# Kernel optimization log

Measured on AMD Instinct MI355X. Metric: run time of the kernel, lower is better.

The kernel has to match this reference:

```python
import jax, jax.numpy as jnp
import numpy as np

B, S, H = 1, 1024, 2048          # batch, seq, hidden_size
I = 7168                          # intermediate_size
E = 8                             # num_local_experts
TOP_K = 2                         # num_experts_per_tok
R = int(I * H * 0.1 / (I + H))    # delta_low_rank = 159
SCALE = 0.02


def setup_inputs() -> dict:
    key = jax.random.key(0)
    ks = jax.random.split(key, 12)
    f = jnp.float32
    return {
        "x": jax.random.normal(ks[0], (B, S, H), dtype=f),
        "gate_w": jax.random.normal(ks[1], (E, H), dtype=f) * SCALE,
        "Wm1": jax.random.normal(ks[2], (I, H), dtype=f) * SCALE,  # Wmean1 (gate proj)
        "Wm2": jax.random.normal(ks[3], (H, I), dtype=f) * SCALE,  # Wmean2 (down proj)
        "Wm3": jax.random.normal(ks[4], (I, H), dtype=f) * SCALE,  # Wmean3 (up proj)
        "du1": jax.random.normal(ks[5], (E, I, R), dtype=f) * SCALE,
        "dv1": jax.random.normal(ks[6], (E, R, H), dtype=f) * SCALE,
        "du2": jax.random.normal(ks[7], (E, H, R), dtype=f) * SCALE,
        "dv2": jax.random.normal(ks[8], (E, R, I), dtype=f) * SCALE,
        "du3": jax.random.normal(ks[9], (E, I, R), dtype=f) * SCALE,
        "dv3": jax.random.normal(ks[10], (E, R, H), dtype=f) * SCALE,
    }


def reference(x, gate_w, Wm1, Wm2, Wm3, du1, dv1, du2, dv2, du3, dv3):
    b, s, h = x.shape
    hs = x.reshape(-1, h)                                  # [T, H]

    # --- router ---
    router_logits = hs @ gate_w.T                          # [T, E]
    probs = jax.nn.softmax(router_logits.astype(jnp.float32), axis=-1)
    top_w, top_i = jax.lax.top_k(probs, TOP_K)             # [T, K]
    top_w = top_w / jnp.sum(top_w, axis=-1, keepdims=True)
    # dense combine weights [T, E]: weight of expert e for token t (0 if not selected)
    comb = jnp.sum(jax.nn.one_hot(top_i, E, dtype=top_w.dtype) * top_w[..., None], axis=1)
    comb = comb.astype(hs.dtype)

    # --- shared mean weights (computed once per token) ---
    base_gate = hs @ Wm1.T                                 # [T, I]
    base_up = hs @ Wm3.T                                   # [T, I]

    # --- per-expert low-rank deltas ---
    t1 = jnp.einsum('th,erh->ter', hs, dv1)                # [T, E, R]
    gate = base_gate[:, None, :] + jnp.einsum('ter,eir->tei', t1, du1)  # [T, E, I]
    t3 = jnp.einsum('th,erh->ter', hs, dv3)
    up = base_up[:, None, :] + jnp.einsum('ter,eir->tei', t3, du3)      # [T, E, I]

    hmid = jax.nn.silu(gate) * up                          # [T, E, I]

    out = jnp.einsum('tei,hi->teh', hmid, Wm2)             # shared down proj
    t2 = jnp.einsum('tei,eri->ter', hmid, dv2)
    out = out + jnp.einsum('ter,ehr->teh', t2, du2)        # [T, E, H]

    final = jnp.einsum('te,teh->th', comb, out).reshape(b, s, h)
    return final, router_logits
```

## Files before the change

### kernel.cpp

```cpp
#include <hip/hip_runtime.h>

#define T_TOK 1024
#define H_DIM 2048
#define I_DIM 7168
#define E_NUM 8
#define R_RANK 159
#define RP 160
#define P_PAIRS 2048

typedef __attribute__((ext_vector_type(8))) short short8;
typedef __attribute__((ext_vector_type(4))) float f32x4;

__device__ __forceinline__ ushort f2b(float f) {
  uint u = __float_as_uint(f);
  uint r = (u + 0x7FFFu + ((u >> 16) & 1u)) >> 16;
  return (ushort)r;
}
__device__ __forceinline__ float b2f(ushort u) {
  return __uint_as_float(((uint)u) << 16);
}
__device__ __forceinline__ short8 pack8(float4 a, float4 b) {
  short8 o;
  o[0] = (short)f2b(a.x); o[1] = (short)f2b(a.y); o[2] = (short)f2b(a.z); o[3] = (short)f2b(a.w);
  o[4] = (short)f2b(b.x); o[5] = (short)f2b(b.y); o[6] = (short)f2b(b.z); o[7] = (short)f2b(b.w);
  return o;
}
__device__ __forceinline__ short8 zero8() {
  short8 z;
#pragma unroll
  for (int q = 0; q < 8; ++q) z[q] = 0;
  return z;
}
__device__ __forceinline__ int swzofs(int row, int g) { return (g ^ ((row >> 1) & 3)) * 8; }

#define GLOAD(gptr, lptr) \
  __builtin_amdgcn_global_load_lds((const __attribute__((address_space(1))) void*)(gptr), \
                                   (__attribute__((address_space(3))) void*)(lptr), 16, 0, 0)

__global__ __launch_bounds__(256) void router_kernel(
    const float* __restrict__ x, const float* __restrict__ gw,
    float* __restrict__ logits, float* __restrict__ comb,
    int* __restrict__ sel_e, int* __restrict__ cnt) {
  int wave = threadIdx.x >> 6, lane = threadIdx.x & 63;
  int t = blockIdx.x * 4 + wave;
  const float* xr = x + (long)t * H_DIM;
  float acc[8] = {0.f,0.f,0.f,0.f,0.f,0.f,0.f,0.f};
  for (int h = lane * 4; h < H_DIM; h += 256) {
    const float4 xv = *(const float4*)&xr[h];
#pragma unroll
    for (int e = 0; e < 8; ++e) {
      const float4 gv = *(const float4*)&gw[e * H_DIM + h];
      acc[e] += xv.x * gv.x + xv.y * gv.y + xv.z * gv.z + xv.w * gv.w;
    }
  }
#pragma unroll
  for (int off = 32; off > 0; off >>= 1)
#pragma unroll
    for (int e = 0; e < 8; ++e) acc[e] += __shfl_down(acc[e], off);
  if (lane == 0) {
#pragma unroll
    for (int e = 0; e < 8; ++e) logits[(long)t * 8 + e] = acc[e];
    int i0 = 0;
    for (int e = 1; e < 8; ++e) if (acc[e] > acc[i0]) i0 = e;
    int i1 = (i0 == 0) ? 1 : 0;
    for (int e = 0; e < 8; ++e) if (e != i0 && acc[e] > acc[i1]) i1 = e;
    float ee = __expf(acc[i1] - acc[i0]);
    float w0 = 1.f / (1.f + ee), w1 = ee / (1.f + ee);
    for (int e = 0; e < 8; ++e) comb[t * 8 + e] = 0.f;
    comb[t * 8 + i0] = w0;
    comb[t * 8 + i1] = w1;
    sel_e[t * 2] = i0;
    sel_e[t * 2 + 1] = i1;
    atomicAdd(&cnt[i0], 1);
    atomicAdd(&cnt[i1], 1);
  }
}

__global__ void init_kernel(int* cnt, int* cursor) {
  int i = threadIdx.x;
  if (i < 8) { cnt[i] = 0; cursor[i] = 0; }
}

__global__ void scan_kernel(const int* cnt, int* seg) {
  if (threadIdx.x == 0) {
    int s = 0;
    for (int e = 0; e < 8; ++e) { seg[e] = s; s += cnt[e]; }
    seg[8] = s;
  }
}

__global__ void assign_kernel(const int* __restrict__ sel_e, const float* __restrict__ comb,
                              const int* __restrict__ seg, int* __restrict__ cursor,
                              int* __restrict__ tok, float* __restrict__ wrow,
                              int* __restrict__ row_of) {
  int t = blockIdx.x * blockDim.x + threadIdx.x;
  if (t >= T_TOK) return;
  for (int k = 0; k < 2; ++k) {
    int e = sel_e[t * 2 + k];
    int pos = atomicAdd(&cursor[e], 1);
    int row = seg[e] + pos;
    tok[row] = t;
    wrow[row] = comb[t * 8 + e];
    row_of[t * 2 + k] = row;
  }
}

__global__ void cast8_kernel(const float* __restrict__ src, ushort* __restrict__ dst, long n8) {
  long idx = (long)blockIdx.x * blockDim.x + threadIdx.x;
  long stride = (long)gridDim.x * blockDim.x;
  for (long i = idx; i < n8; i += stride) {
    const float4 a = *(const float4*)&src[i * 8];
    const float4 b = *(const float4*)&src[i * 8 + 4];
    *(short8*)&dst[i * 8] = pack8(a, b);
  }
}

__global__ void padcast8_kernel(const float* __restrict__ src, ushort* __restrict__ dst, long rows) {
  long n8 = rows * (RP / 8);
  long idx = (long)blockIdx.x * blockDim.x + threadIdx.x;
  long stride = (long)gridDim.x * blockDim.x;
  for (long i = idx; i < n8; i += stride) {
    long row = i / (RP / 8);
    int c0 = (int)(i % (RP / 8)) * 8;
    short8 o;
#pragma unroll
    for (int j = 0; j < 8; ++j) {
      int c = c0 + j;
      o[j] = (c < R_RANK) ? (short)f2b(src[row * R_RANK + c]) : (short)0;
    }
    *(short8*)&dst[row * RP + c0] = o;
  }
}

__global__ void hcomb_kernel(const ushort* __restrict__ hmid, const int* __restrict__ row_of,
                             ushort* __restrict__ hc) {
  long idx = (long)blockIdx.x * blockDim.x + threadIdx.x;
  long total = (long)T_TOK * I_DIM / 8;
  if (idx >= total) return;
  long i = idx * 8;
  int t = (int)(i / I_DIM);
  int col = (int)(i % I_DIM);
  int r0 = row_of[t * 2], r1 = row_of[t * 2 + 1];
  const short8 a = *(const short8*)&hmid[(long)r0 * I_DIM + col];
  const short8 b = *(const short8*)&hmid[(long)r1 * I_DIM + col];
  short8 o;
#pragma unroll
  for (int j = 0; j < 8; ++j)
    o[j] = (short)f2b(b2f((ushort)a[j]) + b2f((ushort)b[j]));
  *(short8*)&hc[i] = o;
}

__global__ void finalfix_kernel(float* __restrict__ out, const ushort* __restrict__ delta,
                                const int* __restrict__ row_of) {
  long idx = (long)blockIdx.x * blockDim.x + threadIdx.x;
  long total = (long)T_TOK * H_DIM / 4;
  if (idx >= total) return;
  long i = idx * 4;
  int t = (int)(i / H_DIM);
  int col = (int)(i % H_DIM);
  int r0 = row_of[t * 2], r1 = row_of[t * 2 + 1];
  float4 d = *(float4*)&out[i];
  d.x += b2f(delta[(long)r0 * H_DIM + col + 0]) + b2f(delta[(long)r1 * H_DIM + col + 0]);
  d.y += b2f(delta[(long)r0 * H_DIM + col + 1]) + b2f(delta[(long)r1 * H_DIM + col + 1]);
  d.z += b2f(delta[(long)r0 * H_DIM + col + 2]) + b2f(delta[(long)r1 * H_DIM + col + 2]);
  d.w += b2f(delta[(long)r0 * H_DIM + col + 3]) + b2f(delta[(long)r1 * H_DIM + col + 3]);
  *(float4*)&out[i] = d;
}

__global__ void finalfixA_kernel(float* __restrict__ out, const float* __restrict__ dp,
                                 const ushort* __restrict__ delta, const int* __restrict__ row_of) {
  long idx = (long)blockIdx.x * blockDim.x + threadIdx.x;
  long total = (long)T_TOK * H_DIM / 4;
  if (idx >= total) return;
  long i = idx * 4;
  int t = (int)(i / H_DIM);
  int col = (int)(i % H_DIM);
  int r0 = row_of[t * 2], r1 = row_of[t * 2 + 1];
  const long plane = (long)T_TOK * H_DIM;
  float4 s = *(const float4*)&dp[i];
#pragma unroll
  for (int k = 1; k < 4; ++k) {
    const float4 q = *(const float4*)&dp[k * plane + i];
    s.x += q.x; s.y += q.y; s.z += q.z; s.w += q.w;
  }
  s.x += b2f(delta[(long)r0 * H_DIM + col + 0]) + b2f(delta[(long)r1 * H_DIM + col + 0]);
  s.y += b2f(delta[(long)r0 * H_DIM + col + 1]) + b2f(delta[(long)r1 * H_DIM + col + 1]);
  s.z += b2f(delta[(long)r0 * H_DIM + col + 2]) + b2f(delta[(long)r1 * H_DIM + col + 2]);
  s.w += b2f(delta[(long)r0 * H_DIM + col + 3]) + b2f(delta[(long)r1 * H_DIM + col + 3]);
  *(float4*)&out[i] = s;
}

template <int KS>
__global__ void reduce_cast_kernel(const float* __restrict__ P, long plane,
                                   ushort* __restrict__ out, long n) {
  long i = (long)blockIdx.x * blockDim.x + threadIdx.x;
  if (i >= n) return;
  float s = 0.f;
#pragma unroll
  for (int k = 0; k < KS; ++k) s += P[(long)k * plane + i];
  out[i] = f2b(s);
}

__global__ void reduce2_kernel(const float* __restrict__ p1, const float* __restrict__ p3,
                               ushort* __restrict__ t1g, ushort* __restrict__ t3g, long n) {
  long i = (long)blockIdx.x * blockDim.x + threadIdx.x;
  if (i >= 2 * n) return;
  const float* P = (i < n) ? p1 : p3;
  ushort* o = (i < n) ? t1g : t3g;
  long ii = (i < n) ? i : i - n;
  float s = 0.f;
#pragma unroll
  for (int k = 0; k < 8; ++k) s += P[(long)k * n + ii];
  o[ii] = f2b(s);
}


__device__ __forceinline__ void kloop32(
    const ushort* ar0, const ushort* ar1,
    const ushort* br0, const ushort* br1,
    int K, ushort* As, ushort* Bs,
    int tid, int lane, int wm, int wn, f32x4 acc[4][4]) {
  for (int k0 = 0; k0 < K; k0 += 32) {
    __syncthreads();
    GLOAD(ar0 + k0, &As[tid * 8]);
    GLOAD(ar1 + k0, &As[(256 + tid) * 8]);
    GLOAD(br0 + k0, &Bs[tid * 8]);
    GLOAD(br1 + k0, &Bs[(256 + tid) * 8]);
    __syncthreads();
    short8 av[4], bv[4];
#pragma unroll
    for (int mi = 0; mi < 4; ++mi) {
      int R = wm + mi * 16 + (lane & 15);
      av[mi] = *(const short8*)&As[R * 32 + swzofs(R, lane >> 4)];
    }
#pragma unroll
    for (int ni = 0; ni < 4; ++ni) {
      int R = wn + ni * 16 + (lane & 15);
      bv[ni] = *(const short8*)&Bs[R * 32 + swzofs(R, lane >> 4)];
    }
#pragma unroll
    for (int mi = 0; mi < 4; ++mi)
#pragma unroll
      for (int ni = 0; ni < 4; ++ni)
        acc[mi][ni] = __builtin_amdgcn_mfma_f32_16x16x32_bf16(av[mi], bv[ni], acc[mi][ni], 0, 0, 0);
  }
}

__device__ __forceinline__ void kloop64(
    const ushort* ar0, const ushort* ar1,
    const ushort* br0, const ushort* br1,
    int K, ushort* As, ushort* Bs,
    int tid, int lane, int wm, int wn, f32x4 acc[4][4]) {
  for (int k0 = 0; k0 < K; k0 += 64) {
    __syncthreads();
    GLOAD(ar0 + k0,      &As[tid * 8]);
    GLOAD(ar1 + k0,      &As[(256 + tid) * 8]);
    GLOAD(ar0 + k0 + 32, &As[4096 + tid * 8]);
    GLOAD(ar1 + k0 + 32, &As[4096 + (256 + tid) * 8]);
    GLOAD(br0 + k0,      &Bs[tid * 8]);
    GLOAD(br1 + k0,      &Bs[(256 + tid) * 8]);
    GLOAD(br0 + k0 + 32, &Bs[4096 + tid * 8]);
    GLOAD(br1 + k0 + 32, &Bs[4096 + (256 + tid) * 8]);
    __syncthreads();
#pragma unroll
    for (int s = 0; s < 2; ++s) {
      short8 av[4], bv[4];
#pragma unroll
      for (int mi = 0; mi < 4; ++mi) {
        int R = wm + mi * 16 + (lane & 15);
        av[mi] = *(const short8*)&As[s * 4096 + R * 32 + swzofs(R, lane >> 4)];
      }
#pragma unroll
      for (int ni = 0; ni < 4; ++ni) {
        int R = wn + ni * 16 + (lane & 15);
        bv[ni] = *(const short8*)&Bs[s * 4096 + R * 32 + swzofs(R, lane >> 4)];
      }
#pragma unroll
      for (int mi = 0; mi < 4; ++mi)
#pragma unroll
        for (int ni = 0; ni < 4; ++ni)
          acc[mi][ni] = __builtin_amdgcn_mfma_f32_16x16x32_bf16(av[mi], bv[ni], acc[mi][ni], 0, 0, 0);
    }
  }
}

__device__ __forceinline__ void epi_bf16(
    f32x4 acc[4][4], ushort* smem, int tid, int lane, int wm, int wn,
    int row0, int col0, int M, int Nvalid, int Npad, ushort* Cb, int ldc) {
  const int er = (lane >> 4) * 4, ec = lane & 15;
  __syncthreads();
#pragma unroll
  for (int mi = 0; mi < 4; ++mi)
#pragma unroll
    for (int ni = 0; ni < 4; ++ni)
#pragma unroll
      for (int j = 0; j < 4; ++j) {
        int rr = wm + mi * 16 + er + j;
        int c = wn + ni * 16 + ec;
        smem[rr * 128 + (c ^ ((rr & 7) << 3))] =
            (col0 + c < Nvalid) ? f2b(acc[mi][ni][j]) : (ushort)0;
      }
  __syncthreads();
  const int rl = tid >> 1, clb = (tid & 1) * 64;
  const int r = row0 + rl;
  if (r < M) {
    const int k8 = (rl & 7) << 3;
#pragma unroll
    for (int jj = 0; jj < 8; ++jj) {
      int cg = col0 + clb + jj * 8;
      if (cg < Npad) {
        short8 v = *(const short8*)&smem[rl * 128 + ((clb + jj * 8) ^ k8)];
        *(short8*)&Cb[(long)r * ldc + cg] = v;
      }
    }
  }
}


__global__ __launch_bounds__(256) void k_base(
    const ushort* __restrict__ xb, const ushort* __restrict__ w1b, const ushort* __restrict__ w3b,
    ushort* __restrict__ bgate, ushort* __restrict__ bup) {
  __shared__ ushort smem[16384];
  ushort* As = smem;
  ushort* Bs = smem + 8192;
  const ushort* B = blockIdx.z ? w3b : w1b;
  ushort* C = blockIdx.z ? bup : bgate;
  const int tid = threadIdx.x;
  const int lane = tid & 63, wave = tid >> 6;
  const int wm = (wave >> 1) * 64, wn = (wave & 1) * 64;
  const int row0 = blockIdx.y * 128, col0 = blockIdx.x * 128;
  const int sub_r = tid >> 2, sub_c = swzofs(sub_r, tid & 3);
  const ushort* ar0 = xb + (long)(row0 + sub_r) * H_DIM + sub_c;
  const ushort* ar1 = xb + (long)(row0 + 64 + sub_r) * H_DIM + sub_c;
  const ushort* br0 = B + (long)(col0 + sub_r) * H_DIM + sub_c;
  const ushort* br1 = B + (long)(col0 + 64 + sub_r) * H_DIM + sub_c;
  f32x4 acc[4][4] = {};
  kloop64(ar0, ar1, br0, br1, H_DIM, As, Bs, tid, lane, wm, wn, acc);
  epi_bf16(acc, smem, tid, lane, wm, wn, row0, col0, T_TOK, I_DIM, I_DIM, C, I_DIM);
}

__global__ __launch_bounds__(256) void k_t13(
    const ushort* __restrict__ xb, const ushort* __restrict__ dv1b, const ushort* __restrict__ dv3b,
    const int* __restrict__ tok, const int* __restrict__ seg, const int* __restrict__ cnt,
    float* __restrict__ p1, float* __restrict__ p3) {
  __shared__ ushort smem[16384];
  ushort* As = smem;
  ushort* Bs = smem + 8192;
  const int z = blockIdx.z;
  const int which = z & 1;
  const int eks = z >> 1;
  const int e = eks >> 3, ks = eks & 7;
  const int m0 = seg[e], M = cnt[e];
  const int row0 = blockIdx.y * 128, col0 = blockIdx.x * 128;
  if (row0 >= M) return;
  const int kbase = ks * 256;
  const ushort* Bsrc = (which ? dv3b : dv1b) + (long)e * R_RANK * H_DIM;
  float* P = which ? p3 : p1;
  const int tid = threadIdx.x;
  const int lane = tid & 63, wave = tid >> 6;
  const int wm = (wave >> 1) * 64, wn = (wave & 1) * 64;
  const int sub_r = tid >> 2, sub_c = swzofs(sub_r, tid & 3);
  int r0c = row0 + sub_r;      if (r0c > M - 1) r0c = M - 1;
  int r1c = row0 + 64 + sub_r; if (r1c > M - 1) r1c = M - 1;
  const ushort* ar0 = xb + (long)tok[m0 + r0c] * H_DIM + kbase + sub_c;
  const ushort* ar1 = xb + (long)tok[m0 + r1c] * H_DIM + kbase + sub_c;
  int q0 = col0 + sub_r;      if (q0 > R_RANK - 1) q0 = R_RANK - 1;
  int q1 = col0 + 64 + sub_r; if (q1 > R_RANK - 1) q1 = R_RANK - 1;
  const ushort* br0 = Bsrc + (long)q0 * H_DIM + kbase + sub_c;
  const ushort* br1 = Bsrc + (long)q1 * H_DIM + kbase + sub_c;
  f32x4 acc[4][4] = {};
  kloop64(ar0, ar1, br0, br1, 256, As, Bs, tid, lane, wm, wn, acc);
  const int er = (lane >> 4) * 4, ec = lane & 15;
  const long plane = (long)P_PAIRS * RP;
#pragma unroll
  for (int mi = 0; mi < 4; ++mi)
#pragma unroll
    for (int ni = 0; ni < 4; ++ni)
#pragma unroll
      for (int j = 0; j < 4; ++j) {
        int r = row0 + wm + mi * 16 + er + j;
        int c = col0 + wn + ni * 16 + ec;
        if (r < M && c < RP)
          P[(long)ks * plane + (long)(m0 + r) * RP + c] = (c < R_RANK) ? acc[mi][ni][j] : 0.f;
      }
}

__global__ __launch_bounds__(256) void k_phase2(
    const ushort* __restrict__ hc, const ushort* __restrict__ w2b,
    const ushort* __restrict__ hmidg, const ushort* __restrict__ dv2b,
    const int* __restrict__ seg, const int* __restrict__ cnt,
    float* __restrict__ dp, float* __restrict__ p2) {
  __shared__ ushort smem[16384];
  ushort* As = smem;
  ushort* Bs = smem + 8192;
  const int tid = threadIdx.x;
  const int lane = tid & 63, wave = tid >> 6;
  const int wm = (wave >> 1) * 64, wn = (wave & 1) * 64;
  const int sub_r = tid >> 2, sub_c = swzofs(sub_r, tid & 3);
  const int er = (lane >> 4) * 4, ec = lane & 15;

  if (blockIdx.z < 4) {
    const int ks = blockIdx.z;
    const int kbase = ks * (I_DIM / 4);
    const int row0 = blockIdx.y * 128, col0 = blockIdx.x * 128;
    const ushort* ar0 = hc + (long)(row0 + sub_r) * I_DIM + kbase + sub_c;
    const ushort* ar1 = hc + (long)(row0 + 64 + sub_r) * I_DIM + kbase + sub_c;
    const ushort* br0 = w2b + (long)(col0 + sub_r) * I_DIM + kbase + sub_c;
    const ushort* br1 = w2b + (long)(col0 + 64 + sub_r) * I_DIM + kbase + sub_c;
    f32x4 acc[4][4] = {};
    kloop64(ar0, ar1, br0, br1, I_DIM / 4, As, Bs, tid, lane, wm, wn, acc);
    float* Pk = dp + (long)ks * T_TOK * H_DIM;
#pragma unroll
    for (int mi = 0; mi < 4; ++mi)
#pragma unroll
      for (int ni = 0; ni < 4; ++ni)
#pragma unroll
        for (int j = 0; j < 4; ++j) {
          int r = row0 + wm + mi * 16 + er + j;
          int c = col0 + wn + ni * 16 + ec;
          Pk[(long)r * H_DIM + c] = acc[mi][ni][j];
        }
  } else {
    const int f = (blockIdx.z - 4) * 128 + blockIdx.y * 16 + blockIdx.x;
    const int eks = f >> 4;
    const int e = eks >> 3, ks = eks & 7;
    const int rsub = f & 15;
    const int x2 = rsub & 1, y2 = rsub >> 1;
    const int m0 = seg[e], M = cnt[e];
    const int row0 = y2 * 128, col0 = x2 * 128;
    if (row0 >= M) return;
    const int kbase = ks * (I_DIM / 8);
    int r0c = row0 + sub_r;      if (r0c > M - 1) r0c = M - 1;
    int r1c = row0 + 64 + sub_r; if (r1c > M - 1) r1c = M - 1;
    const ushort* ar0 = hmidg + (long)(m0 + r0c) * I_DIM + kbase + sub_c;
    const ushort* ar1 = hmidg + (long)(m0 + r1c) * I_DIM + kbase + sub_c;
    int q0 = col0 + sub_r;      if (q0 > R_RANK - 1) q0 = R_RANK - 1;
    int q1 = col0 + 64 + sub_r; if (q1 > R_RANK - 1) q1 = R_RANK - 1;
    const ushort* br0 = dv2b + (long)e * R_RANK * I_DIM + (long)q0 * I_DIM + kbase + sub_c;
    const ushort* br1 = dv2b + (long)e * R_RANK * I_DIM + (long)q1 * I_DIM + kbase + sub_c;
    f32x4 acc[4][4] = {};
    kloop64(ar0, ar1, br0, br1, I_DIM / 8, As, Bs, tid, lane, wm, wn, acc);
    const long plane = (long)P_PAIRS * RP;
#pragma unroll
    for (int mi = 0; mi < 4; ++mi)
#pragma unroll
      for (int ni = 0; ni < 4; ++ni)
#pragma unroll
        for (int j = 0; j < 4; ++j) {
          int r = row0 + wm + mi * 16 + er + j;
          int c = col0 + wn + ni * 16 + ec;
          if (r < M && c < RP)
            p2[(long)ks * plane + (long)(m0 + r) * RP + c] = (c < R_RANK) ? acc[mi][ni][j] : 0.f;
        }
  }
}

__global__ __launch_bounds__(256) void k_delta(
    const ushort* __restrict__ t2g, const ushort* __restrict__ du2b,
    const int* __restrict__ seg, const int* __restrict__ cnt,
    ushort* __restrict__ deltab) {
  __shared__ ushort smem[16384];
  ushort* As = smem;
  ushort* Bs = smem + 4096;
  const int e = blockIdx.z;
  const int m0 = seg[e], M = cnt[e];
  const int row0 = blockIdx.y * 128, col0 = blockIdx.x * 128;
  if (row0 >= M) return;
  const int tid = threadIdx.x;
  const int lane = tid & 63, wave = tid >> 6;
  const int wm = (wave >> 1) * 64, wn = (wave & 1) * 64;
  const int sub_r = tid >> 2, sub_c = swzofs(sub_r, tid & 3);
  int r0c = row0 + sub_r;      if (r0c > M - 1) r0c = M - 1;
  int r1c = row0 + 64 + sub_r; if (r1c > M - 1) r1c = M - 1;
  const ushort* ar0 = t2g + (long)(m0 + r0c) * RP + sub_c;
  const ushort* ar1 = t2g + (long)(m0 + r1c) * RP + sub_c;
  const ushort* br0 = du2b + (long)e * H_DIM * RP + (long)(col0 + sub_r) * RP + sub_c;
  const ushort* br1 = du2b + (long)e * H_DIM * RP + (long)(col0 + 64 + sub_r) * RP + sub_c;
  f32x4 acc[4][4] = {};
  kloop32(ar0, ar1, br0, br1, RP, As, Bs, tid, lane, wm, wn, acc);
  epi_bf16(acc, smem, tid, lane, wm, wn, row0, col0, M, H_DIM, H_DIM,
           deltab + (long)m0 * H_DIM, H_DIM);
}

__global__ __launch_bounds__(256) void gemm_hmid(
    const ushort* __restrict__ t1g, const ushort* __restrict__ t3g,
    const ushort* __restrict__ du1b, const ushort* __restrict__ du3b,
    const ushort* __restrict__ bgate, const ushort* __restrict__ bup,
    const int* __restrict__ tok, const float* __restrict__ wrow,
    const int* __restrict__ seg, const int* __restrict__ cnt,
    ushort* __restrict__ hmid) {
  __shared__ ushort smem[16384];
  ushort* As1 = smem;
  ushort* As3 = smem + 4096;
  ushort* Bs1 = smem + 8192;
  ushort* Bs3 = smem + 12288;
  int e = blockIdx.z;
  int m0 = seg[e], M = cnt[e];
  if ((int)(blockIdx.y * 128) >= M) return;
  const ushort* A1 = t1g + (long)m0 * RP;
  const ushort* A3 = t3g + (long)m0 * RP;
  const ushort* B1 = du1b + (long)e * I_DIM * RP;
  const ushort* B3 = du3b + (long)e * I_DIM * RP;
  tok += m0; wrow += m0;
  ushort* H = hmid + (long)m0 * I_DIM;

  const int tid = threadIdx.x;
  const int lane = tid & 63, wave = tid >> 6;
  const int wm = (wave >> 1) * 64, wn = (wave & 1) * 64;
  const int row0 = blockIdx.y * 128, col0 = blockIdx.x * 128;
  const int sub_r = tid >> 2;
  const int sub_c = swzofs(sub_r, tid & 3);

  const ushort *a1r[2], *a3r[2], *b1r[2], *b3r[2];
#pragma unroll
  for (int p = 0; p < 2; ++p) {
    int r = row0 + p * 64 + sub_r; if (r > M - 1) r = M - 1;
    a1r[p] = A1 + (long)r * RP + sub_c;
    a3r[p] = A3 + (long)r * RP + sub_c;
    int q = col0 + p * 64 + sub_r; if (q > I_DIM - 1) q = I_DIM - 1;
    b1r[p] = B1 + (long)q * RP + sub_c;
    b3r[p] = B3 + (long)q * RP + sub_c;
  }

  f32x4 acc1[4][4] = {}, acc3[4][4] = {};

  for (int k0 = 0; k0 < RP; k0 += 32) {
    __syncthreads();
#pragma unroll
    for (int p = 0; p < 2; ++p) {
      GLOAD(a1r[p] + k0, &As1[(p * 256 + tid) * 8]);
      GLOAD(a3r[p] + k0, &As3[(p * 256 + tid) * 8]);
      GLOAD(b1r[p] + k0, &Bs1[(p * 256 + tid) * 8]);
      GLOAD(b3r[p] + k0, &Bs3[(p * 256 + tid) * 8]);
    }
    __syncthreads();

    short8 av1[4], av3[4], bv1[4], bv3[4];
#pragma unroll
    for (int mi = 0; mi < 4; ++mi) {
      int R = wm + mi * 16 + (lane & 15);
      int o = R * 32 + swzofs(R, lane >> 4);
      av1[mi] = *(const short8*)&As1[o];
      av3[mi] = *(const short8*)&As3[o];
    }
#pragma unroll
    for (int ni = 0; ni < 4; ++ni) {
      int R = wn + ni * 16 + (lane & 15);
      int o = R * 32 + swzofs(R, lane >> 4);
      bv1[ni] = *(const short8*)&Bs1[o];
      bv3[ni] = *(const short8*)&Bs3[o];
    }
#pragma unroll
    for (int mi = 0; mi < 4; ++mi)
#pragma unroll
      for (int ni = 0; ni < 4; ++ni) {
        acc1[mi][ni] = __builtin_amdgcn_mfma_f32_16x16x32_bf16(av1[mi], bv1[ni], acc1[mi][ni], 0, 0, 0);
        acc3[mi][ni] = __builtin_amdgcn_mfma_f32_16x16x32_bf16(av3[mi], bv3[ni], acc3[mi][ni], 0, 0, 0);
      }
  }

  const int er = (lane >> 4) * 4;
  const int ec = lane & 15;
  __syncthreads();
  ushort* Cs = smem;
#pragma unroll
  for (int mi = 0; mi < 4; ++mi)
#pragma unroll
    for (int ni = 0; ni < 4; ++ni)
#pragma unroll
      for (int j = 0; j < 4; ++j) {
        int rr = wm + mi * 16 + er + j;
        int c = wn + ni * 16 + ec;
        Cs[rr * 128 + (c ^ ((rr & 7) << 3))] = f2b(acc1[mi][ni][j]);
      }
  __syncthreads();
  const int rl = tid >> 1;
  const int clb = (tid & 1) * 64;
  const int r = row0 + rl;
  const bool rok = (r < M);
  const int t = rok ? tok[r] : 0;
  const float w = rok ? wrow[r] : 0.f;
  const int k8 = (rl & 7) << 3;
  uint svp[32];
#pragma unroll
  for (int jj = 0; jj < 8; ++jj) {
    short8 gb = zero8();
    if (rok) gb = *(const short8*)&bgate[(long)t * I_DIM + col0 + clb + jj * 8];
    short8 gv = *(const short8*)&Cs[rl * 128 + ((clb + jj * 8) ^ k8)];
#pragma unroll
    for (int q = 0; q < 8; q += 2) {
      float g0 = b2f((ushort)gv[q]) + b2f((ushort)gb[q]);
      float g1 = b2f((ushort)gv[q + 1]) + b2f((ushort)gb[q + 1]);
      float s0 = g0 / (1.f + __expf(-g0));
      float s1 = g1 / (1.f + __expf(-g1));
      svp[jj * 4 + q / 2] = (uint)f2b(s0) | ((uint)f2b(s1) << 16);
    }
  }
  __syncthreads();
#pragma unroll
  for (int mi = 0; mi < 4; ++mi)
#pragma unroll
    for (int ni = 0; ni < 4; ++ni)
#pragma unroll
      for (int j = 0; j < 4; ++j) {
        int rr = wm + mi * 16 + er + j;
        int c = wn + ni * 16 + ec;
        Cs[rr * 128 + (c ^ ((rr & 7) << 3))] = f2b(acc3[mi][ni][j]);
      }
  __syncthreads();
#pragma unroll
  for (int jj = 0; jj < 8; ++jj) {
    short8 ub = zero8();
    if (rok) ub = *(const short8*)&bup[(long)t * I_DIM + col0 + clb + jj * 8];
    short8 uv = *(const short8*)&Cs[rl * 128 + ((clb + jj * 8) ^ k8)];
    short8 o;
#pragma unroll
    for (int q = 0; q < 8; q += 2) {
      uint sp = svp[jj * 4 + q / 2];
      float u0 = b2f((ushort)uv[q]) + b2f((ushort)ub[q]);
      float u1 = b2f((ushort)uv[q + 1]) + b2f((ushort)ub[q + 1]);
      o[q]     = (short)f2b(w * b2f((ushort)(sp & 0xFFFFu)) * u0);
      o[q + 1] = (short)f2b(w * b2f((ushort)(sp >> 16)) * u1);
    }
    if (rok) *(short8*)&H[(long)r * I_DIM + col0 + clb + jj * 8] = o;
  }
}

template <int AF32, int BF32, int CBF16, int PEREXP, int AMAP>
__global__ __launch_bounds__(256) void gemm_f(
    const void* __restrict__ Ap, int lda,
    const void* __restrict__ Bp, int ldb, long Bstride,
    int M, int N, int K, int Npad,
    float* __restrict__ Cf, ushort* __restrict__ Cb, int ldc,
    const int* __restrict__ tok, const int* __restrict__ seg, const int* __restrict__ cnt) {
  __shared__ ushort smem[16384];
  ushort* As = smem;
  ushort* Bs = smem + 4096;
  const float* Af = (const float*)Ap;
  const ushort* Ab = (const ushort*)Ap;
  const float* Bf = (const float*)Bp;
  const ushort* Bb = (const ushort*)Bp;
  const int* amap = tok;
  if (PEREXP) {
    int e = blockIdx.z;
    int m0 = seg[e];
    M = cnt[e];
    if ((int)(blockIdx.y * 128) >= M) return;
    if (AMAP) {
      amap = tok + m0;
    } else {
      if (AF32) Af += (long)m0 * lda; else Ab += (long)m0 * lda;
    }
    if (BF32) Bf += (long)e * Bstride; else Bb += (long)e * Bstride;
    if (CBF16) Cb += (long)m0 * ldc; else Cf += (long)m0 * ldc;
  }
  const int tid = threadIdx.x;
  const int lane = tid & 63, wave = tid >> 6;
  const int wm = (wave >> 1) * 64, wn = (wave & 1) * 64;
  const int row0 = blockIdx.y * 128, col0 = blockIdx.x * 128;
  const int sub_r = tid >> 2;
  const int sub_c = (tid & 3) * 8;

  const float* afrow[2]; const ushort* abrow[2];
  const float* bfrow[2]; const ushort* bbrow[2];
#pragma unroll
  for (int p = 0; p < 2; ++p) {
    int r = row0 + p * 64 + sub_r; if (r > M - 1) r = M - 1;
    if (AMAP) r = amap[r];
    if (AF32) afrow[p] = Af + (long)r * lda + sub_c;
    else      abrow[p] = Ab + (long)r * lda + sub_c;
    int q = col0 + p * 64 + sub_r; if (q > N - 1) q = N - 1;
    if (BF32) bfrow[p] = Bf + (long)q * ldb + sub_c;
    else      bbrow[p] = Bb + (long)q * ldb + sub_c;
  }

  f32x4 acc[4][4] = {};

  for (int k0 = 0; k0 < K; k0 += 32) {
    float4 a0[2], a1[2], b0[2], b1[2];
    if (AF32) {
#pragma unroll
      for (int p = 0; p < 2; ++p) {
        a0[p] = *(const float4*)(afrow[p] + k0);
        a1[p] = *(const float4*)(afrow[p] + k0 + 4);
      }
    }
    if (BF32) {
#pragma unroll
      for (int p = 0; p < 2; ++p) {
        b0[p] = *(const float4*)(bfrow[p] + k0);
        b1[p] = *(const float4*)(bfrow[p] + k0 + 4);
      }
    }
    __syncthreads();
#pragma unroll
    for (int p = 0; p < 2; ++p) {
      if (AF32) {
        *(short8*)&As[(p * 256 + tid) * 8] = pack8(a0[p], a1[p]);
      } else {
        GLOAD(abrow[p] + k0, &As[(p * 256 + tid) * 8]);
      }
      if (BF32) {
        *(short8*)&Bs[(p * 256 + tid) * 8] = pack8(b0[p], b1[p]);
      } else {
        GLOAD(bbrow[p] + k0, &Bs[(p * 256 + tid) * 8]);
      }
    }
    __syncthreads();

    short8 av[4], bv[4];
#pragma unroll
    for (int mi = 0; mi < 4; ++mi)
      av[mi] = *(const short8*)&As[(wm + mi * 16 + (lane & 15)) * 32 + (lane >> 4) * 8];
#pragma unroll
    for (int ni = 0; ni < 4; ++ni)
      bv[ni] = *(const short8*)&Bs[(wn + ni * 16 + (lane & 15)) * 32 + (lane >> 4) * 8];
#pragma unroll
    for (int mi = 0; mi < 4; ++mi)
#pragma unroll
      for (int ni = 0; ni < 4; ++ni)
        acc[mi][ni] = __builtin_amdgcn_mfma_f32_16x16x32_bf16(av[mi], bv[ni], acc[mi][ni], 0, 0, 0);
  }

  const int er = (lane >> 4) * 4;
  const int ec = lane & 15;
  if (CBF16) {
    __syncthreads();
    ushort* Cs = smem;
#pragma unroll
    for (int mi = 0; mi < 4; ++mi)
#pragma unroll
      for (int ni = 0; ni < 4; ++ni)
#pragma unroll
        for (int j = 0; j < 4; ++j) {
          int rr = wm + mi * 16 + er + j;
          int c = wn + ni * 16 + ec;
          Cs[rr * 128 + (c ^ ((rr & 7) << 3))] =
              (col0 + c < N) ? f2b(acc[mi][ni][j]) : (ushort)0;
        }
    __syncthreads();
    const int rl = tid >> 1;
    const int clb = (tid & 1) * 64;
    const int r = row0 + rl;
    if (r < M) {
      const int k8 = (rl & 7) << 3;
#pragma unroll
      for (int jj = 0; jj < 8; ++jj) {
        int cg = col0 + clb + jj * 8;
        if (cg < Npad) {
          short8 v = *(const short8*)&Cs[rl * 128 + ((clb + jj * 8) ^ k8)];
          *(short8*)&Cb[(long)r * ldc + cg] = v;
        }
      }
    }
  } else {
#pragma unroll
    for (int mi = 0; mi < 4; ++mi)
#pragma unroll
      for (int ni = 0; ni < 4; ++ni)
#pragma unroll
        for (int j = 0; j < 4; ++j) {
          int r = row0 + wm + mi * 16 + er + j;
          int c = col0 + wn + ni * 16 + ec;
          if (r < M && c < Npad)
            Cf[(long)r * ldc + c] = (c < N) ? acc[mi][ni][j] : 0.f;
        }
  }
}

extern "C" void kernel_launch(void* const* d_in, const int* in_sizes, int n_in,
                              void* d_out, int out_size, void* d_ws, size_t ws_size,
                              hipStream_t stream) {
  const float* x   = (const float*)d_in[0];
  const float* gw  = (const float*)d_in[1];
  const float* Wm1 = (const float*)d_in[2];
  const float* Wm2 = (const float*)d_in[3];
  const float* Wm3 = (const float*)d_in[4];
  const float* du1 = (const float*)d_in[5];
  const float* dv1 = (const float*)d_in[6];
  const float* du2 = (const float*)d_in[7];
  const float* dv2 = (const float*)d_in[8];
  const float* du3 = (const float*)d_in[9];
  const float* dv3 = (const float*)d_in[10];

  float* out_final  = (float*)d_out;
  float* out_logits = out_final + (long)T_TOK * H_DIM;

  char* p = (char*)d_ws;
  auto alloc = [&](size_t bytes) {
    char* r = p;
    p += (bytes + 255) & ~(size_t)255;
    return r;
  };

  float* comb   = (float*)alloc((size_t)T_TOK * E_NUM * 4);
  float* wrow   = (float*)alloc((size_t)P_PAIRS * 4);
  int* cnt      = (int*)alloc(64);
  int* cursor   = (int*)alloc(64);
  int* seg      = (int*)alloc(64);
  int* sel_e    = (int*)alloc((size_t)T_TOK * 2 * 4);
  int* tok      = (int*)alloc((size_t)P_PAIRS * 4);
  int* row_of   = (int*)alloc((size_t)T_TOK * 2 * 4);
  ushort* bgate_b = (ushort*)alloc((size_t)T_TOK * I_DIM * 2);
  ushort* bup_b   = (ushort*)alloc((size_t)T_TOK * I_DIM * 2);
  ushort* hmidg   = (ushort*)alloc((size_t)P_PAIRS * I_DIM * 2);
  ushort* t1g     = (ushort*)alloc((size_t)P_PAIRS * RP * 2);
  ushort* t3g     = (ushort*)alloc((size_t)P_PAIRS * RP * 2);
  ushort* t2g     = (ushort*)alloc((size_t)P_PAIRS * RP * 2);
  ushort* du1b    = (ushort*)alloc((size_t)E_NUM * I_DIM * RP * 2);
  ushort* du3b    = (ushort*)alloc((size_t)E_NUM * I_DIM * RP * 2);
  ushort* du2b    = (ushort*)alloc((size_t)E_NUM * H_DIM * RP * 2);
  size_t needed_B = (size_t)(p - (char*)d_ws);
  ushort* xb   = (ushort*)alloc((size_t)T_TOK * H_DIM * 2);
  ushort* w1b  = (ushort*)alloc((size_t)I_DIM * H_DIM * 2);
  ushort* w3b  = (ushort*)alloc((size_t)I_DIM * H_DIM * 2);
  ushort* dv1b = (ushort*)alloc((size_t)E_NUM * R_RANK * H_DIM * 2);
  ushort* dv3b = (ushort*)alloc((size_t)E_NUM * R_RANK * H_DIM * 2);
  size_t needed_A = (size_t)(p - (char*)d_ws);
  ushort* w2b_d  = (ushort*)alloc((size_t)I_DIM * H_DIM * 2);
  ushort* dv2b_d = (ushort*)alloc((size_t)E_NUM * R_RANK * I_DIM * 2);
  size_t needed_A2 = (size_t)(p - (char*)d_ws);

  ushort* hc     = bgate_b;
  ushort* deltab = bup_b;

  if (ws_size < needed_B) return;
  const bool planA  = (ws_size >= needed_A);
  const bool planA2 = (ws_size >= needed_A2);

  dim3 blk(256);

  init_kernel<<<1, 64, 0, stream>>>(cnt, cursor);
  router_kernel<<<T_TOK / 4, 256, 0, stream>>>(x, gw, out_logits, comb, sel_e, cnt);
  scan_kernel<<<1, 64, 0, stream>>>(cnt, seg);
  assign_kernel<<<4, 256, 0, stream>>>(sel_e, comb, seg, cursor, tok, wrow, row_of);

  padcast8_kernel<<<4480, 256, 0, stream>>>(du1, du1b, (long)E_NUM * I_DIM);
  padcast8_kernel<<<4480, 256, 0, stream>>>(du3, du3b, (long)E_NUM * I_DIM);
  padcast8_kernel<<<1280, 256, 0, stream>>>(du2, du2b, (long)E_NUM * H_DIM);

  if (planA) {
    ushort* w2b  = planA2 ? w2b_d  : w1b;
    ushort* dv2b = planA2 ? dv2b_d : w3b;

    cast8_kernel<<<1024, 256, 0, stream>>>(x, xb, (long)T_TOK * H_DIM / 8);
    cast8_kernel<<<7168, 256, 0, stream>>>(Wm1, w1b, (long)I_DIM * H_DIM / 8);
    cast8_kernel<<<7168, 256, 0, stream>>>(Wm3, w3b, (long)I_DIM * H_DIM / 8);
    cast8_kernel<<<1272, 256, 0, stream>>>(dv1, dv1b, (long)E_NUM * R_RANK * H_DIM / 8);
    cast8_kernel<<<1272, 256, 0, stream>>>(dv3, dv3b, (long)E_NUM * R_RANK * H_DIM / 8);
    if (planA2) {
      cast8_kernel<<<7168, 256, 0, stream>>>(Wm2, w2b, (long)I_DIM * H_DIM / 8);
      cast8_kernel<<<4452, 256, 0, stream>>>(dv2, dv2b, (long)E_NUM * R_RANK * I_DIM / 8);
    }

    k_base<<<dim3(I_DIM / 128, T_TOK / 128, 2), blk, 0, stream>>>(xb, w1b, w3b, bgate_b, bup_b);

    float* p1 = (float*)hmidg;
    float* p3 = p1 + (long)8 * P_PAIRS * RP;
    k_t13<<<dim3(2, 8, 128), blk, 0, stream>>>(xb, dv1b, dv3b, tok, seg, cnt, p1, p3);
    reduce2_kernel<<<2560, 256, 0, stream>>>(p1, p3, t1g, t3g, (long)P_PAIRS * RP);

    if (!planA2) {
      cast8_kernel<<<7168, 256, 0, stream>>>(Wm2, w2b, (long)I_DIM * H_DIM / 8);
      cast8_kernel<<<4452, 256, 0, stream>>>(dv2, dv2b, (long)E_NUM * R_RANK * I_DIM / 8);
    }

    gemm_hmid<<<dim3(I_DIM / 128, 8, E_NUM), blk, 0, stream>>>(
        t1g, t3g, du1b, du3b, bgate_b, bup_b, tok, wrow, seg, cnt, hmidg);

    hcomb_kernel<<<(int)(((long)T_TOK * I_DIM / 8 + 255) / 256), 256, 0, stream>>>(hmidg, row_of, hc);

    float* dp = (float*)du1b;
    float* p2 = (float*)bup_b;
    k_phase2<<<dim3(H_DIM / 128, 8, 12), blk, 0, stream>>>(
        hc, w2b, hmidg, dv2b, seg, cnt, dp, p2);
    reduce_cast_kernel<8><<<1280, 256, 0, stream>>>(p2, (long)P_PAIRS * RP, t2g, (long)P_PAIRS * RP);

    k_delta<<<dim3(H_DIM / 128, 8, E_NUM), blk, 0, stream>>>(t2g, du2b, seg, cnt, deltab);

    finalfixA_kernel<<<2048, 256, 0, stream>>>(out_final, dp, deltab, row_of);
  } else {
    gemm_f<1, 1, 1, 0, 0><<<dim3(I_DIM / 128, T_TOK / 128, 1), blk, 0, stream>>>(
        x, H_DIM, Wm1, H_DIM, 0L, T_TOK, I_DIM, H_DIM, I_DIM,
        nullptr, bgate_b, I_DIM, nullptr, nullptr, nullptr);
    gemm_f<1, 1, 1, 0, 0><<<dim3(I_DIM / 128, T_TOK / 128, 1), blk, 0, stream>>>(
        x, H_DIM, Wm3, H_DIM, 0L, T_TOK, I_DIM, H_DIM, I_DIM,
        nullptr, bup_b, I_DIM, nullptr, nullptr, nullptr);
    gemm_f<1, 1, 1, 1, 1><<<dim3(2, 8, E_NUM), blk, 0, stream>>>(
        x, H_DIM, dv1, H_DIM, (long)R_RANK * H_DIM, 0, R_RANK, H_DIM, RP,
        nullptr, t1g, RP, tok, seg, cnt);
    gemm_f<1, 1, 1, 1, 1><<<dim3(2, 8, E_NUM), blk, 0, stream>>>(
        x, H_DIM, dv3, H_DIM, (long)R_RANK * H_DIM, 0, R_RANK, H_DIM, RP,
        nullptr, t3g, RP, tok, seg, cnt);
    gemm_hmid<<<dim3(I_DIM / 128, 8, E_NUM), blk, 0, stream>>>(
        t1g, t3g, du1b, du3b, bgate_b, bup_b, tok, wrow, seg, cnt, hmidg);
    hcomb_kernel<<<(int)(((long)T_TOK * I_DIM / 8 + 255) / 256), 256, 0, stream>>>(hmidg, row_of, hc);
    gemm_f<0, 1, 0, 0, 0><<<dim3(H_DIM / 128, T_TOK / 128, 1), blk, 0, stream>>>(
        hc, I_DIM, Wm2, I_DIM, 0L, T_TOK, H_DIM, I_DIM, H_DIM,
        out_final, nullptr, H_DIM, nullptr, nullptr, nullptr);
    gemm_f<0, 1, 1, 1, 0><<<dim3(2, 8, E_NUM), blk, 0, stream>>>(
        hmidg, I_DIM, dv2, I_DIM, (long)R_RANK * I_DIM, 0, R_RANK, I_DIM, RP,
        nullptr, t2g, RP, tok, seg, cnt);
    gemm_f<0, 0, 1, 1, 0><<<dim3(H_DIM / 128, 8, E_NUM), blk, 0, stream>>>(
        t2g, RP, du2b, RP, (long)H_DIM * RP, 0, H_DIM, RP, H_DIM,
        nullptr, deltab, H_DIM, tok, seg, cnt);
    finalfix_kernel<<<(int)(((long)T_TOK * H_DIM / 4 + 255) / 256), 256, 0, stream>>>(
        out_final, deltab, row_of);
  }
}
```

Baseline: 500.9 us.

## Merge cast launches into megacast, fuse base and t13 GEMMs, trim padded rank tiles

```diff
diff --git a/kernel.cpp b/kernel.cpp
--- a/kernel.cpp
+++ b/kernel.cpp
@@ -7,6 +7,13 @@
 #define R_RANK 159
 #define RP 160
 #define P_PAIRS 2048
+
+#define CH_X    262144L
+#define CH_W    1835008L
+#define CH_DV13 325632L
+#define CH_DV2  1139712L
+#define CH_DU13 1146880L
+#define CH_DU2  327680L
 
 typedef __attribute__((ext_vector_type(8))) short short8;
 typedef __attribute__((ext_vector_type(4))) float f32x4;
@@ -105,13 +112,54 @@
   }
 }
 
-__global__ void cast8_kernel(const float* __restrict__ src, ushort* __restrict__ dst, long n8) {
-  long idx = (long)blockIdx.x * blockDim.x + threadIdx.x;
-  long stride = (long)gridDim.x * blockDim.x;
-  for (long i = idx; i < n8; i += stride) {
-    const float4 a = *(const float4*)&src[i * 8];
-    const float4 b = *(const float4*)&src[i * 8 + 4];
-    *(short8*)&dst[i * 8] = pack8(a, b);
+__device__ __forceinline__ void castchunk(const float* __restrict__ s, ushort* __restrict__ d, long c) {
+  const float4 a = *(const float4*)&s[c * 8];
+  const float4 b = *(const float4*)&s[c * 8 + 4];
+  *(short8*)&d[c * 8] = pack8(a, b);
+}
+__device__ __forceinline__ void padchunk(const float* __restrict__ s, ushort* __restrict__ d, long c) {
+  long row = c / 20;
+  int c0 = (int)(c % 20) * 8;
+  short8 o;
+#pragma unroll
+  for (int j = 0; j < 8; ++j) {
+    int cc = c0 + j;
+    o[j] = (cc < R_RANK) ? (short)f2b(s[row * R_RANK + cc]) : (short)0;
+  }
+  *(short8*)&d[row * RP + c0] = o;
+}
+
+__global__ void megacast_kernel(
+    const float* __restrict__ x, const float* __restrict__ Wm1, const float* __restrict__ Wm3,
+    const float* __restrict__ dv1, const float* __restrict__ dv3,
+    const float* __restrict__ du1, const float* __restrict__ du3, const float* __restrict__ du2,
+    ushort* __restrict__ xb, ushort* __restrict__ w1b, ushort* __restrict__ w3b,
+    ushort* __restrict__ dv1b, ushort* __restrict__ dv3b,
+    ushort* __restrict__ du1b, ushort* __restrict__ du3b, ushort* __restrict__ du2b) {
+  const long TOT = CH_W * 2 + CH_DU13 * 2 + CH_DU2 + CH_DV13 * 2 + CH_X;
+  for (long c0 = (long)blockIdx.x * blockDim.x + threadIdx.x; c0 < TOT;
+       c0 += (long)gridDim.x * blockDim.x) {
+    long c = c0;
+    if (c < CH_W)    { castchunk(Wm1, w1b, c); continue; }  c -= CH_W;
+    if (c < CH_W)    { castchunk(Wm3, w3b, c); continue; }  c -= CH_W;
+    if (c < CH_DU13) { padchunk(du1, du1b, c); continue; }  c -= CH_DU13;
+    if (c < CH_DU13) { padchunk(du3, du3b, c); continue; }  c -= CH_DU13;
+    if (c < CH_DU2)  { padchunk(du2, du2b, c); continue; }  c -= CH_DU2;
+    if (c < CH_DV13) { castchunk(dv1, dv1b, c); continue; } c -= CH_DV13;
+    if (c < CH_DV13) { castchunk(dv3, dv3b, c); continue; } c -= CH_DV13;
+    castchunk(x, xb, c);
+  }
+}
+
+__global__ void cast2_kernel(const float* __restrict__ Wm2, const float* __restrict__ dv2,
+                             ushort* __restrict__ w2b, ushort* __restrict__ dv2b) {
+  const long TOT = CH_W + CH_DV2;
+  for (long c0 = (long)blockIdx.x * blockDim.x + threadIdx.x; c0 < TOT;
+       c0 += (long)gridDim.x * blockDim.x) {
+    long c = c0;
+    if (c < CH_W) { castchunk(Wm2, w2b, c); continue; }
+    c -= CH_W;
+    castchunk(dv2, dv2b, c);
   }
 }
 
@@ -119,17 +167,7 @@
   long n8 = rows * (RP / 8);
   long idx = (long)blockIdx.x * blockDim.x + threadIdx.x;
   long stride = (long)gridDim.x * blockDim.x;
-  for (long i = idx; i < n8; i += stride) {
-    long row = i / (RP / 8);
-    int c0 = (int)(i % (RP / 8)) * 8;
-    short8 o;
-#pragma unroll
-    for (int j = 0; j < 8; ++j) {
-      int c = c0 + j;
-      o[j] = (c < R_RANK) ? (short)f2b(src[row * R_RANK + c]) : (short)0;
-    }
-    *(short8*)&dst[row * RP + c0] = o;
-  }
+  for (long i = idx; i < n8; i += stride) padchunk(src, dst, i);
 }
 
 __global__ void hcomb_kernel(const ushort* __restrict__ hmid, const int* __restrict__ row_of,
@@ -246,39 +284,43 @@
   }
 }
 
-__device__ __forceinline__ void kloop64(
+template <int NI>
+__device__ __forceinline__ void kloop64t(
     const ushort* ar0, const ushort* ar1,
     const ushort* br0, const ushort* br1,
     int K, ushort* As, ushort* Bs,
     int tid, int lane, int wm, int wn, f32x4 acc[4][4]) {
+  const int sub_r = tid >> 2;
   for (int k0 = 0; k0 < K; k0 += 64) {
     __syncthreads();
     GLOAD(ar0 + k0,      &As[tid * 8]);
     GLOAD(ar1 + k0,      &As[(256 + tid) * 8]);
     GLOAD(ar0 + k0 + 32, &As[4096 + tid * 8]);
     GLOAD(ar1 + k0 + 32, &As[4096 + (256 + tid) * 8]);
-    GLOAD(br0 + k0,      &Bs[tid * 8]);
-    GLOAD(br1 + k0,      &Bs[(256 + tid) * 8]);
-    GLOAD(br0 + k0 + 32, &Bs[4096 + tid * 8]);
-    GLOAD(br1 + k0 + 32, &Bs[4096 + (256 + tid) * 8]);
+    if (NI == 4 || sub_r < 32) {
+      GLOAD(br0 + k0,      &Bs[tid * 8]);
+      GLOAD(br1 + k0,      &Bs[(256 + tid) * 8]);
+      GLOAD(br0 + k0 + 32, &Bs[4096 + tid * 8]);
+      GLOAD(br1 + k0 + 32, &Bs[4096 + (256 + tid) * 8]);
+    }
     __syncthreads();
 #pragma unroll
     for (int s = 0; s < 2; ++s) {
-      short8 av[4], bv[4];
+      short8 av[4], bv[NI];
 #pragma unroll
       for (int mi = 0; mi < 4; ++mi) {
         int R = wm + mi * 16 + (lane & 15);
         av[mi] = *(const short8*)&As[s * 4096 + R * 32 + swzofs(R, lane >> 4)];
       }
 #pragma unroll
-      for (int ni = 0; ni < 4; ++ni) {
+      for (int ni = 0; ni < NI; ++ni) {
         int R = wn + ni * 16 + (lane & 15);
         bv[ni] = *(const short8*)&Bs[s * 4096 + R * 32 + swzofs(R, lane >> 4)];
       }
 #pragma unroll
       for (int mi = 0; mi < 4; ++mi)
 #pragma unroll
-        for (int ni = 0; ni < 4; ++ni)
+        for (int ni = 0; ni < NI; ++ni)
           acc[mi][ni] = __builtin_amdgcn_mfma_f32_16x16x32_bf16(av[mi], bv[ni], acc[mi][ni], 0, 0, 0);
     }
   }
@@ -317,72 +359,73 @@
 }
 
 
-__global__ __launch_bounds__(256) void k_base(
+__global__ __launch_bounds__(256) void k_early(
     const ushort* __restrict__ xb, const ushort* __restrict__ w1b, const ushort* __restrict__ w3b,
-    ushort* __restrict__ bgate, ushort* __restrict__ bup) {
-  __shared__ ushort smem[16384];
-  ushort* As = smem;
-  ushort* Bs = smem + 8192;
-  const ushort* B = blockIdx.z ? w3b : w1b;
-  ushort* C = blockIdx.z ? bup : bgate;
-  const int tid = threadIdx.x;
-  const int lane = tid & 63, wave = tid >> 6;
-  const int wm = (wave >> 1) * 64, wn = (wave & 1) * 64;
-  const int row0 = blockIdx.y * 128, col0 = blockIdx.x * 128;
-  const int sub_r = tid >> 2, sub_c = swzofs(sub_r, tid & 3);
-  const ushort* ar0 = xb + (long)(row0 + sub_r) * H_DIM + sub_c;
-  const ushort* ar1 = xb + (long)(row0 + 64 + sub_r) * H_DIM + sub_c;
-  const ushort* br0 = B + (long)(col0 + sub_r) * H_DIM + sub_c;
-  const ushort* br1 = B + (long)(col0 + 64 + sub_r) * H_DIM + sub_c;
-  f32x4 acc[4][4] = {};
-  kloop64(ar0, ar1, br0, br1, H_DIM, As, Bs, tid, lane, wm, wn, acc);
-  epi_bf16(acc, smem, tid, lane, wm, wn, row0, col0, T_TOK, I_DIM, I_DIM, C, I_DIM);
-}
-
-__global__ __launch_bounds__(256) void k_t13(
-    const ushort* __restrict__ xb, const ushort* __restrict__ dv1b, const ushort* __restrict__ dv3b,
+    const ushort* __restrict__ dv1b, const ushort* __restrict__ dv3b,
     const int* __restrict__ tok, const int* __restrict__ seg, const int* __restrict__ cnt,
+    ushort* __restrict__ bgate, ushort* __restrict__ bup,
     float* __restrict__ p1, float* __restrict__ p3) {
   __shared__ ushort smem[16384];
   ushort* As = smem;
   ushort* Bs = smem + 8192;
-  const int z = blockIdx.z;
-  const int which = z & 1;
-  const int eks = z >> 1;
-  const int e = eks >> 3, ks = eks & 7;
-  const int m0 = seg[e], M = cnt[e];
-  const int row0 = blockIdx.y * 128, col0 = blockIdx.x * 128;
-  if (row0 >= M) return;
-  const int kbase = ks * 256;
-  const ushort* Bsrc = (which ? dv3b : dv1b) + (long)e * R_RANK * H_DIM;
-  float* P = which ? p3 : p1;
+  const int b = blockIdx.x;
   const int tid = threadIdx.x;
   const int lane = tid & 63, wave = tid >> 6;
   const int wm = (wave >> 1) * 64, wn = (wave & 1) * 64;
   const int sub_r = tid >> 2, sub_c = swzofs(sub_r, tid & 3);
-  int r0c = row0 + sub_r;      if (r0c > M - 1) r0c = M - 1;
-  int r1c = row0 + 64 + sub_r; if (r1c > M - 1) r1c = M - 1;
-  const ushort* ar0 = xb + (long)tok[m0 + r0c] * H_DIM + kbase + sub_c;
-  const ushort* ar1 = xb + (long)tok[m0 + r1c] * H_DIM + kbase + sub_c;
-  int q0 = col0 + sub_r;      if (q0 > R_RANK - 1) q0 = R_RANK - 1;
-  int q1 = col0 + 64 + sub_r; if (q1 > R_RANK - 1) q1 = R_RANK - 1;
-  const ushort* br0 = Bsrc + (long)q0 * H_DIM + kbase + sub_c;
-  const ushort* br1 = Bsrc + (long)q1 * H_DIM + kbase + sub_c;
-  f32x4 acc[4][4] = {};
-  kloop64(ar0, ar1, br0, br1, 256, As, Bs, tid, lane, wm, wn, acc);
-  const int er = (lane >> 4) * 4, ec = lane & 15;
-  const long plane = (long)P_PAIRS * RP;
-#pragma unroll
-  for (int mi = 0; mi < 4; ++mi)
-#pragma unroll
-    for (int ni = 0; ni < 4; ++ni)
-#pragma unroll
-      for (int j = 0; j < 4; ++j) {
-        int r = row0 + wm + mi * 16 + er + j;
-        int c = col0 + wn + ni * 16 + ec;
-        if (r < M && c < RP)
-          P[(long)ks * plane + (long)(m0 + r) * RP + c] = (c < R_RANK) ? acc[mi][ni][j] : 0.f;
-      }
+
+  if (b < 896) {
+    const int z = b / 448, r448 = b % 448;
+    const int xk = r448 % 56, yk = r448 / 56;
+    const int row0 = yk * 128, col0 = xk * 128;
+    const ushort* B = z ? w3b : w1b;
+    ushort* C = z ? bup : bgate;
+    const ushort* ar0 = xb + (long)(row0 + sub_r) * H_DIM + sub_c;
+    const ushort* ar1 = xb + (long)(row0 + 64 + sub_r) * H_DIM + sub_c;
+    const ushort* br0 = B + (long)(col0 + sub_r) * H_DIM + sub_c;
+    const ushort* br1 = B + (long)(col0 + 64 + sub_r) * H_DIM + sub_c;
+    f32x4 acc[4][4] = {};
+    kloop64t<4>(ar0, ar1, br0, br1, H_DIM, As, Bs, tid, lane, wm, wn, acc);
+    epi_bf16(acc, smem, tid, lane, wm, wn, row0, col0, T_TOK, I_DIM, I_DIM, C, I_DIM);
+  } else {
+    const int f = b - 896;
+    const int xk = f & 1, yk = (f >> 1) & 7, zk = f >> 4;
+    const int which = zk & 1;
+    const int eks = zk >> 1;
+    const int e = eks >> 3, ks = eks & 7;
+    const int m0 = seg[e], M = cnt[e];
+    const int row0 = yk * 128, col0 = xk * 128;
+    if (row0 >= M) return;
+    const int kbase = ks * 256;
+    const ushort* Bsrc = (which ? dv3b : dv1b) + (long)e * R_RANK * H_DIM;
+    float* P = which ? p3 : p1;
+    int r0c = row0 + sub_r;      if (r0c > M - 1) r0c = M - 1;
+    int r1c = row0 + 64 + sub_r; if (r1c > M - 1) r1c = M - 1;
+    const ushort* ar0 = xb + (long)tok[m0 + r0c] * H_DIM + kbase + sub_c;
+    const ushort* ar1 = xb + (long)tok[m0 + r1c] * H_DIM + kbase + sub_c;
+    int q0 = col0 + sub_r;      if (q0 > R_RANK - 1) q0 = R_RANK - 1;
+    int q1 = col0 + 64 + sub_r; if (q1 > R_RANK - 1) q1 = R_RANK - 1;
+    const ushort* br0 = Bsrc + (long)q0 * H_DIM + kbase + sub_c;
+    const ushort* br1 = Bsrc + (long)q1 * H_DIM + kbase + sub_c;
+    f32x4 acc[4][4] = {};
+    if (xk == 0)
+      kloop64t<4>(ar0, ar1, br0, br1, 256, As, Bs, tid, lane, wm, wn, acc);
+    else
+      kloop64t<2>(ar0, ar1, br0, br1, 256, As, Bs, tid, lane, wm, wn, acc);
+    const int er = (lane >> 4) * 4, ec = lane & 15;
+    const long plane = (long)P_PAIRS * RP;
+#pragma unroll
+    for (int mi = 0; mi < 4; ++mi)
+#pragma unroll
+      for (int ni = 0; ni < 4; ++ni)
+#pragma unroll
+        for (int j = 0; j < 4; ++j) {
+          int r = row0 + wm + mi * 16 + er + j;
+          int c = col0 + wn + ni * 16 + ec;
+          if (r < M && c < RP)
+            P[(long)ks * plane + (long)(m0 + r) * RP + c] = (c < R_RANK) ? acc[mi][ni][j] : 0.f;
+        }
+  }
 }
 
 __global__ __launch_bounds__(256) void k_phase2(
@@ -408,7 +451,7 @@
     const ushort* br0 = w2b + (long)(col0 + sub_r) * I_DIM + kbase + sub_c;
     const ushort* br1 = w2b + (long)(col0 + 64 + sub_r) * I_DIM + kbase + sub_c;
     f32x4 acc[4][4] = {};
-    kloop64(ar0, ar1, br0, br1, I_DIM / 4, As, Bs, tid, lane, wm, wn, acc);
+    kloop64t<4>(ar0, ar1, br0, br1, I_DIM / 4, As, Bs, tid, lane, wm, wn, acc);
     float* Pk = dp + (long)ks * T_TOK * H_DIM;
 #pragma unroll
     for (int mi = 0; mi < 4; ++mi)
@@ -439,7 +482,10 @@
     const ushort* br0 = dv2b + (long)e * R_RANK * I_DIM + (long)q0 * I_DIM + kbase + sub_c;
     const ushort* br1 = dv2b + (long)e * R_RANK * I_DIM + (long)q1 * I_DIM + kbase + sub_c;
     f32x4 acc[4][4] = {};
-    kloop64(ar0, ar1, br0, br1, I_DIM / 8, As, Bs, tid, lane, wm, wn, acc);
+    if (x2 == 0)
+      kloop64t<4>(ar0, ar1, br0, br1, I_DIM / 8, As, Bs, tid, lane, wm, wn, acc);
+    else
+      kloop64t<2>(ar0, ar1, br0, br1, I_DIM / 8, As, Bs, tid, lane, wm, wn, acc);
     const long plane = (long)P_PAIRS * RP;
 #pragma unroll
     for (int mi = 0; mi < 4; ++mi)
@@ -835,35 +881,23 @@
   scan_kernel<<<1, 64, 0, stream>>>(cnt, seg);
   assign_kernel<<<4, 256, 0, stream>>>(sel_e, comb, seg, cursor, tok, wrow, row_of);
 
-  padcast8_kernel<<<4480, 256, 0, stream>>>(du1, du1b, (long)E_NUM * I_DIM);
-  padcast8_kernel<<<4480, 256, 0, stream>>>(du3, du3b, (long)E_NUM * I_DIM);
-  padcast8_kernel<<<1280, 256, 0, stream>>>(du2, du2b, (long)E_NUM * H_DIM);
-
   if (planA) {
     ushort* w2b  = planA2 ? w2b_d  : w1b;
     ushort* dv2b = planA2 ? dv2b_d : w3b;
 
-    cast8_kernel<<<1024, 256, 0, stream>>>(x, xb, (long)T_TOK * H_DIM / 8);
-    cast8_kernel<<<7168, 256, 0, stream>>>(Wm1, w1b, (long)I_DIM * H_DIM / 8);
-    cast8_kernel<<<7168, 256, 0, stream>>>(Wm3, w3b, (long)I_DIM * H_DIM / 8);
-    cast8_kernel<<<1272, 256, 0, stream>>>(dv1, dv1b, (long)E_NUM * R_RANK * H_DIM / 8);
-    cast8_kernel<<<1272, 256, 0, stream>>>(dv3, dv3b, (long)E_NUM * R_RANK * H_DIM / 8);
-    if (planA2) {
-      cast8_kernel<<<7168, 256, 0, stream>>>(Wm2, w2b, (long)I_DIM * H_DIM / 8);
-      cast8_kernel<<<4452, 256, 0, stream>>>(dv2, dv2b, (long)E_NUM * R_RANK * I_DIM / 8);
-    }
-
-    k_base<<<dim3(I_DIM / 128, T_TOK / 128, 2), blk, 0, stream>>>(xb, w1b, w3b, bgate_b, bup_b);
+    megacast_kernel<<<2048, 256, 0, stream>>>(x, Wm1, Wm3, dv1, dv3, du1, du3, du2,
+                                              xb, w1b, w3b, dv1b, dv3b, du1b, du3b, du2b);
+    if (planA2)
+      cast2_kernel<<<1024, 256, 0, stream>>>(Wm2, dv2, w2b, dv2b);
 
     float* p1 = (float*)hmidg;
     float* p3 = p1 + (long)8 * P_PAIRS * RP;
-    k_t13<<<dim3(2, 8, 128), blk, 0, stream>>>(xb, dv1b, dv3b, tok, seg, cnt, p1, p3);
+    k_early<<<2944, blk, 0, stream>>>(xb, w1b, w3b, dv1b, dv3b, tok, seg, cnt,
+                                      bgate_b, bup_b, p1, p3);
     reduce2_kernel<<<2560, 256, 0, stream>>>(p1, p3, t1g, t3g, (long)P_PAIRS * RP);
 
-    if (!planA2) {
-      cast8_kernel<<<7168, 256, 0, stream>>>(Wm2, w2b, (long)I_DIM * H_DIM / 8);
-      cast8_kernel<<<4452, 256, 0, stream>>>(dv2, dv2b, (long)E_NUM * R_RANK * I_DIM / 8);
-    }
+    if (!planA2)
+      cast2_kernel<<<1024, 256, 0, stream>>>(Wm2, dv2, w2b, dv2b);
 
     gemm_hmid<<<dim3(I_DIM / 128, 8, E_NUM), blk, 0, stream>>>(
         t1g, t3g, du1b, du3b, bgate_b, bup_b, tok, wrow, seg, cnt, hmidg);
@@ -880,6 +914,9 @@
 
     finalfixA_kernel<<<2048, 256, 0, stream>>>(out_final, dp, deltab, row_of);
   } else {
+    padcast8_kernel<<<4480, 256, 0, stream>>>(du1, du1b, (long)E_NUM * I_DIM);
+    padcast8_kernel<<<4480, 256, 0, stream>>>(du3, du3b, (long)E_NUM * I_DIM);
+    padcast8_kernel<<<1280, 256, 0, stream>>>(du2, du2b, (long)E_NUM * H_DIM);
     gemm_f<1, 1, 1, 0, 0><<<dim3(I_DIM / 128, T_TOK / 128, 1), blk, 0, stream>>>(
         x, H_DIM, Wm1, H_DIM, 0L, T_TOK, I_DIM, H_DIM, I_DIM,
         nullptr, bgate_b, I_DIM, nullptr, nullptr, nullptr);
```

Measured after the change: 480.1 us. -4.2%, faster.
